# Performance work log

Measured on AMD Instinct MI355X. Metric: run time of the kernel, lower is better.

The kernel has to match this reference:

```python
import jax, jax.numpy as jnp
import numpy as np

B, H, W, C = 4, 256, 256, 256
WS = 8          # window size (both dims)
HEADS = 1
SEQ = WS * WS   # 64 tokens per window
NW = B * (H // WS) * (W // WS)  # 4096 windows
INNER = C * HEADS


def setup_inputs() -> dict:
    key = jax.random.key(0)
    k1, k2, k3, k4 = jax.random.split(key, 4)
    x = jax.random.normal(k1, (B, H, W, C), dtype=jnp.float32)
    attn = jax.random.uniform(k2, (NW, HEADS, SEQ, SEQ), dtype=jnp.float32)
    # to_v: Linear(dim, inner_dim, bias=False); stored as [in, out] for x @ Wv
    Wv = jax.random.normal(k3, (C, INNER), dtype=jnp.float32) * (C ** -0.5)
    # to_out: Linear(inner_dim, dim)
    Wo = jax.random.normal(k4, (INNER, C), dtype=jnp.float32) * (INNER ** -0.5)
    bo = jnp.zeros((C,), dtype=jnp.float32)
    return {"x": x, "attn": attn, "Wv": Wv, "Wo": Wo, "bo": bo}


def reference(x, attn, Wv, Wo, bo):
    b, h, w, c = x.shape
    nh, nw = h // WS, w // WS
    # window partition: b (h b0) (w b1) c -> (b h w) (b0 b1) c
    xw = x.reshape(b, nh, WS, nw, WS, c).transpose(0, 1, 3, 2, 4, 5)
    xw = xw.reshape(b * nh * nw, SEQ, c)
    # value projection, split heads: n s (h d) -> n h s d
    v = (xw @ Wv).reshape(-1, SEQ, HEADS, c).transpose(0, 2, 1, 3)
    # precomputed-attention weighted sum
    out = jnp.einsum('nhij,nhjd->nhid', attn, v)
    # merge heads: n h s d -> n s (h d)
    out = out.transpose(0, 2, 1, 3).reshape(-1, SEQ, HEADS * c)
    out = out @ Wo + bo
    # window un-partition: (b h w) (b0 b1) c -> b (h b0) (w b1) c
    out = out.reshape(b, nh, nw, WS, WS, c).transpose(0, 1, 3, 2, 4, 5)
    return out.reshape(b, h, w, c)
```

## Files before the change

### kernel.cpp

```cpp
#include <hip/hip_runtime.h>
#include <hip/hip_bf16.h>


typedef __bf16 bf16x8 __attribute__((ext_vector_type(8)));
typedef __bf16 bf16x4 __attribute__((ext_vector_type(4)));
typedef float  f32x16 __attribute__((ext_vector_type(16)));
typedef float  f32x4  __attribute__((ext_vector_type(4)));
typedef unsigned int uint;
typedef uint   uint4v __attribute__((ext_vector_type(4)));

#define MFMA32(a, b, c) __builtin_amdgcn_mfma_f32_32x32x16_bf16(a, b, c, 0, 0, 0)

__global__ void wfuse_kernel(const float* __restrict__ Wv,
                             const float* __restrict__ Wo,
                             __bf16* __restrict__ WT) {
  const int n = blockIdx.x;
  const int k = threadIdx.x;
  const float* wvrow = Wv + k * 256;
  float acc = 0.f;
#pragma unroll 4
  for (int j = 0; j < 256; j += 4) {
    f32x4 wv = *(const f32x4*)(wvrow + j);
    acc += wv.x * Wo[(j + 0) * 256 + n];
    acc += wv.y * Wo[(j + 1) * 256 + n];
    acc += wv.z * Wo[(j + 2) * 256 + n];
    acc += wv.w * Wo[(j + 3) * 256 + n];
  }
  WT[n * 256 + k] = (__bf16)acc;
}

static __device__ __forceinline__ uint pkbf(float lo, float hi) {
  return (uint)__builtin_bit_cast(unsigned short, (__bf16)lo) |
         ((uint)__builtin_bit_cast(unsigned short, (__bf16)hi) << 16);
}

static __device__ __forceinline__ void build_bfrags(const f32x16 acc, int lh,
                                                    bf16x8* bf) {
  uint wd0 = pkbf(acc[0],  acc[1]);
  uint wd1 = pkbf(acc[2],  acc[3]);
  uint wd2 = pkbf(acc[4],  acc[5]);
  uint wd3 = pkbf(acc[6],  acc[7]);
  uint wd4 = pkbf(acc[8],  acc[9]);
  uint wd5 = pkbf(acc[10], acc[11]);
  uint wd6 = pkbf(acc[12], acc[13]);
  uint wd7 = pkbf(acc[14], acc[15]);
  {
    uint o0 = (uint)__shfl_xor((int)wd2, 32);
    uint o1 = (uint)__shfl_xor((int)wd3, 32);
    uint o2 = (uint)__shfl_xor((int)wd0, 32);
    uint o3 = (uint)__shfl_xor((int)wd1, 32);
    uint4v uv = { lh ? o0 : wd0, lh ? o1 : wd1,
                  lh ? wd2 : o2, lh ? wd3 : o3 };
    bf[0] = __builtin_bit_cast(bf16x8, uv);
  }
  {
    uint o0 = (uint)__shfl_xor((int)wd6, 32);
    uint o1 = (uint)__shfl_xor((int)wd7, 32);
    uint o2 = (uint)__shfl_xor((int)wd4, 32);
    uint o3 = (uint)__shfl_xor((int)wd5, 32);
    uint4v uv = { lh ? o0 : wd4, lh ? o1 : wd5,
                  lh ? wd6 : o2, lh ? wd7 : o3 };
    bf[1] = __builtin_bit_cast(bf16x8, uv);
  }
}

static __device__ __forceinline__ long wbase(int w) {
  int wi = w & 31;
  int hi = (w >> 5) & 31;
  int b  = w >> 10;
  return (((long)(b * 256 + hi * 8)) * 256 + wi * 8) * 256;
}

__global__ __launch_bounds__(512)
__attribute__((amdgpu_waves_per_eu(4, 4)))
void na_msa_kernel(const float* __restrict__ x,
                   const float* __restrict__ attn,
                   const __bf16* __restrict__ WT,
                   const float* __restrict__ bo,
                   float* __restrict__ out) {
  __shared__ char lds[81920];

  const int t    = threadIdx.x;
  const int lane = t & 63;
  const int wvi  = t >> 6;
  const int ln31 = lane & 31;
  const int lh   = lane >> 5;

  const int tq   = t >> 6;
  const int xch0 = (t & 63) * 4;
  const int arow0 = t >> 4;
  const int ak0  = (t & 15) * 4;

  const __bf16* wtp = WT + (wvi * 32 + ln31) * 256 + 8 * lh;
  const float bv = bo[wvi * 32 + ln31];

  const int w0 = blockIdx.x * 4;

#define XBYT(J)  ((((J) * 8 + tq) * 512) + ((xch0 * 2) ^ (((((J) * 8 + tq)) & 31) << 4)))
#define ABYT(I)  (((I) * 32 + arow0) * 128 + ((ak0 * 2) ^ ((((I) * 32 + arow0) & 7) << 4)))
#define CVT4(V)  bf16x4{ (__bf16)(V).x, (__bf16)(V).y, (__bf16)(V).z, (__bf16)(V).w }

  {
    const float* xp = x + wbase(w0);
    const float* ap = attn + (long)w0 * 4096;
    f32x4 v0 = *(const f32x4*)(xp + 0 * 65536 + t * 4);
    f32x4 v1 = *(const f32x4*)(xp + 1 * 65536 + t * 4);
    f32x4 v2 = *(const f32x4*)(xp + 2 * 65536 + t * 4);
    f32x4 v3 = *(const f32x4*)(xp + 3 * 65536 + t * 4);
    f32x4 v4 = *(const f32x4*)(xp + 4 * 65536 + t * 4);
    f32x4 v5 = *(const f32x4*)(xp + 5 * 65536 + t * 4);
    f32x4 v6 = *(const f32x4*)(xp + 6 * 65536 + t * 4);
    f32x4 v7 = *(const f32x4*)(xp + 7 * 65536 + t * 4);
    f32x4 a0 = *(const f32x4*)(ap + t * 4);
    f32x4 a1 = *(const f32x4*)(ap + (512 + t) * 4);
    *(bf16x4*)(lds + XBYT(0)) = CVT4(v0);
    *(bf16x4*)(lds + XBYT(1)) = CVT4(v1);
    *(bf16x4*)(lds + XBYT(2)) = CVT4(v2);
    *(bf16x4*)(lds + XBYT(3)) = CVT4(v3);
    *(bf16x4*)(lds + XBYT(4)) = CVT4(v4);
    *(bf16x4*)(lds + XBYT(5)) = CVT4(v5);
    *(bf16x4*)(lds + XBYT(6)) = CVT4(v6);
    *(bf16x4*)(lds + XBYT(7)) = CVT4(v7);
    *(bf16x4*)(lds + 32768 + ABYT(0)) = CVT4(a0);
    *(bf16x4*)(lds + 32768 + ABYT(1)) = CVT4(a1);
  }
  asm volatile("s_waitcnt lgkmcnt(0)" ::: "memory");
  __builtin_amdgcn_s_barrier();
  __builtin_amdgcn_sched_barrier(0);

#pragma unroll 1
  for (int i = 0; i < 4; ++i) {
    const int w = w0 + i;
    char* lds_xw = lds + (i & 1) * 40960;
    char* lds_at = lds_xw + 32768;

    f32x4 px0, px1, px2, px3, px4, px5, px6, px7, pa0, pa1;
    if (i < 3) {
      const float* xp = x + wbase(w + 1);
      const float* ap = attn + (long)(w + 1) * 4096;
      px0 = *(const f32x4*)(xp + 0 * 65536 + t * 4);
      px1 = *(const f32x4*)(xp + 1 * 65536 + t * 4);
      px2 = *(const f32x4*)(xp + 2 * 65536 + t * 4);
      px3 = *(const f32x4*)(xp + 3 * 65536 + t * 4);
      px4 = *(const f32x4*)(xp + 4 * 65536 + t * 4);
      px5 = *(const f32x4*)(xp + 5 * 65536 + t * 4);
      px6 = *(const f32x4*)(xp + 6 * 65536 + t * 4);
      px7 = *(const f32x4*)(xp + 7 * 65536 + t * 4);
      pa0 = *(const f32x4*)(ap + t * 4);
      pa1 = *(const f32x4*)(ap + (512 + t) * 4);
    }
    __builtin_amdgcn_sched_barrier(0);

    f32x16 acc0 = {}, acc1 = {};
#pragma unroll 2
    for (int ks = 0; ks < 16; ++ks) {
      int kk = ks * 16 + 8 * lh;
      int byt0 = ln31 * 512 + ((kk * 2) ^ (ln31 << 4));
      bf16x8 a0 = *(const bf16x8*)(lds_xw + byt0);
      bf16x8 a1 = *(const bf16x8*)(lds_xw + byt0 + 16384);
      bf16x8 b0 = *(const bf16x8*)(wtp + ks * 16);
      acc0 = MFMA32(a0, b0, acc0);
      acc1 = MFMA32(a1, b0, acc1);
    }
    __builtin_amdgcn_sched_barrier(0);

    bf16x8 bfr[4];
    build_bfrags(acc0, lh, &bfr[0]);
    build_bfrags(acc1, lh, &bfr[2]);

    if (i < 3) {
      char* bxw = lds + ((i + 1) & 1) * 40960;
      char* bat = bxw + 32768;
      *(bf16x4*)(bxw + XBYT(0)) = CVT4(px0);
      *(bf16x4*)(bxw + XBYT(1)) = CVT4(px1);
      *(bf16x4*)(bxw + XBYT(2)) = CVT4(px2);
      *(bf16x4*)(bxw + XBYT(3)) = CVT4(px3);
      *(bf16x4*)(bxw + XBYT(4)) = CVT4(px4);
      *(bf16x4*)(bxw + XBYT(5)) = CVT4(px5);
      *(bf16x4*)(bxw + XBYT(6)) = CVT4(px6);
      *(bf16x4*)(bxw + XBYT(7)) = CVT4(px7);
      *(bf16x4*)(bat + ABYT(0)) = CVT4(pa0);
      *(bf16x4*)(bat + ABYT(1)) = CVT4(pa1);
    }

    f32x16 o0 = {}, o1 = {};
#pragma unroll
    for (int ks = 0; ks < 4; ++ks) {
      int kk = ks * 16 + 8 * lh;
      int ab0 = ln31 * 128 + ((kk * 2) ^ ((ln31 & 7) << 4));
      bf16x8 a0 = *(const bf16x8*)(lds_at + ab0);
      bf16x8 a1 = *(const bf16x8*)(lds_at + ab0 + 4096);
      o0 = MFMA32(a0, bfr[ks], o0);
      o1 = MFMA32(a1, bfr[ks], o1);
    }

    {
      float* op = out + wbase(w);
      const int ch = wvi * 32 + ln31;
#pragma unroll
      for (int r = 0; r < 16; ++r) {
        int tok = (r & 3) + 8 * (r >> 2) + 4 * lh;
        op[(tok >> 3) * 65536 + (tok & 7) * 256 + ch] = o0[r] + bv;
      }
#pragma unroll
      for (int r = 0; r < 16; ++r) {
        int tok = 32 + (r & 3) + 8 * (r >> 2) + 4 * lh;
        op[(tok >> 3) * 65536 + (tok & 7) * 256 + ch] = o1[r] + bv;
      }
    }

    asm volatile("s_waitcnt lgkmcnt(0)" ::: "memory");
    __builtin_amdgcn_s_barrier();
    __builtin_amdgcn_sched_barrier(0);
  }
}

extern "C" void kernel_launch(void* const* d_in, const int* in_sizes, int n_in,
                              void* d_out, int out_size, void* d_ws, size_t ws_size,
                              hipStream_t stream) {
  const float* x    = (const float*)d_in[0];
  const float* attn = (const float*)d_in[1];
  const float* Wv   = (const float*)d_in[2];
  const float* Wo   = (const float*)d_in[3];
  const float* bo   = (const float*)d_in[4];
  float* out = (float*)d_out;
  __bf16* WT = (__bf16*)d_ws;

  wfuse_kernel<<<256, 256, 0, stream>>>(Wv, Wo, WT);
  na_msa_kernel<<<1024, 512, 0, stream>>>(x, attn, WT, bo, out);
}
```

Before: 180.9 us.

## Hoist fused weights into registers and process 16 windows per block

```diff
diff --git a/kernel.cpp b/kernel.cpp
--- a/kernel.cpp
+++ b/kernel.cpp
@@ -71,8 +71,7 @@
   return (((long)(b * 256 + hi * 8)) * 256 + wi * 8) * 256;
 }
 
-__global__ __launch_bounds__(512)
-__attribute__((amdgpu_waves_per_eu(4, 4)))
+__global__ __launch_bounds__(512, 2)
 void na_msa_kernel(const float* __restrict__ x,
                    const float* __restrict__ attn,
                    const __bf16* __restrict__ WT,
@@ -86,19 +85,30 @@
   const int ln31 = lane & 31;
   const int lh   = lane >> 5;
 
+  const __bf16* wtp = WT + (wvi * 32 + ln31) * 256 + 8 * lh;
+  const float bv = bo[wvi * 32 + ln31];
+
   const int tq   = t >> 6;
   const int xch0 = (t & 63) * 4;
   const int arow0 = t >> 4;
-  const int ak0  = (t & 15) * 4;
-
-  const __bf16* wtp = WT + (wvi * 32 + ln31) * 256 + 8 * lh;
-  const float bv = bo[wvi * 32 + ln31];
-
-  const int w0 = blockIdx.x * 4;
-
-#define XBYT(J)  ((((J) * 8 + tq) * 512) + ((xch0 * 2) ^ (((((J) * 8 + tq)) & 31) << 4)))
-#define ABYT(I)  (((I) * 32 + arow0) * 128 + ((ak0 * 2) ^ ((((I) * 32 + arow0) & 7) << 4)))
+  const int ak0   = (t & 15) * 4;
+
+  const int w0 = blockIdx.x * 16;
+
+#define XBYT(J)  ((((J) * 8 + tq) * 512) + ((xch0 * 2) ^ ((((J) * 8 + tq) & 31) << 4)))
 #define CVT4(V)  bf16x4{ (__bf16)(V).x, (__bf16)(V).y, (__bf16)(V).z, (__bf16)(V).w }
+
+#define AWR(BAT, R0, R1) do {                                              \
+    *(bf16x4*)((BAT) + arow0 * 128 + ((ak0 * 2) ^ ((arow0 & 7) << 4))) =   \
+        bf16x4{ (__bf16)(R0).x, (__bf16)(R0).y, (__bf16)(R0).z, (__bf16)(R0).w }; \
+    int row1_ = 32 + arow0;                                                \
+    *(bf16x4*)((BAT) + row1_ * 128 + ((ak0 * 2) ^ ((row1_ & 7) << 4))) =   \
+        bf16x4{ (__bf16)(R1).x, (__bf16)(R1).y, (__bf16)(R1).z, (__bf16)(R1).w }; \
+    } while (0)
+
+  bf16x8 wb[16];
+#pragma unroll
+  for (int ks = 0; ks < 16; ++ks) wb[ks] = *(const bf16x8*)(wtp + ks * 16);
 
   {
     const float* xp = x + wbase(w0);
@@ -121,21 +131,20 @@
     *(bf16x4*)(lds + XBYT(5)) = CVT4(v5);
     *(bf16x4*)(lds + XBYT(6)) = CVT4(v6);
     *(bf16x4*)(lds + XBYT(7)) = CVT4(v7);
-    *(bf16x4*)(lds + 32768 + ABYT(0)) = CVT4(a0);
-    *(bf16x4*)(lds + 32768 + ABYT(1)) = CVT4(a1);
+    AWR(lds + 32768, a0, a1);
   }
   asm volatile("s_waitcnt lgkmcnt(0)" ::: "memory");
   __builtin_amdgcn_s_barrier();
   __builtin_amdgcn_sched_barrier(0);
 
 #pragma unroll 1
-  for (int i = 0; i < 4; ++i) {
+  for (int i = 0; i < 16; ++i) {
     const int w = w0 + i;
-    char* lds_xw = lds + (i & 1) * 40960;
-    char* lds_at = lds_xw + 32768;
+    const char* xs = lds + (i & 1) * 40960;
+    const char* as = xs + 32768;
 
     f32x4 px0, px1, px2, px3, px4, px5, px6, px7, pa0, pa1;
-    if (i < 3) {
+    if (i < 15) {
       const float* xp = x + wbase(w + 1);
       const float* ap = attn + (long)(w + 1) * 4096;
       px0 = *(const f32x4*)(xp + 0 * 65536 + t * 4);
@@ -152,25 +161,56 @@
     __builtin_amdgcn_sched_barrier(0);
 
     f32x16 acc0 = {}, acc1 = {};
-#pragma unroll 2
+#pragma unroll
     for (int ks = 0; ks < 16; ++ks) {
       int kk = ks * 16 + 8 * lh;
       int byt0 = ln31 * 512 + ((kk * 2) ^ (ln31 << 4));
-      bf16x8 a0 = *(const bf16x8*)(lds_xw + byt0);
-      bf16x8 a1 = *(const bf16x8*)(lds_xw + byt0 + 16384);
-      bf16x8 b0 = *(const bf16x8*)(wtp + ks * 16);
-      acc0 = MFMA32(a0, b0, acc0);
-      acc1 = MFMA32(a1, b0, acc1);
-    }
-    __builtin_amdgcn_sched_barrier(0);
+      bf16x8 a0 = *(const bf16x8*)(xs + byt0);
+      bf16x8 a1 = *(const bf16x8*)(xs + byt0 + 16384);
+      acc0 = MFMA32(a0, wb[ks], acc0);
+      acc1 = MFMA32(a1, wb[ks], acc1);
+    }
 
     bf16x8 bfr[4];
     build_bfrags(acc0, lh, &bfr[0]);
     build_bfrags(acc1, lh, &bfr[2]);
 
-    if (i < 3) {
+    float* op = out + wbase(w);
+    const int ch = wvi * 32 + ln31;
+
+    {
+      f32x16 o0 = {};
+#pragma unroll
+      for (int ks = 0; ks < 4; ++ks) {
+        int kk = ks * 16 + 8 * lh;
+        int ab0 = ln31 * 128 + ((kk * 2) ^ ((ln31 & 7) << 4));
+        bf16x8 a0 = *(const bf16x8*)(as + ab0);
+        o0 = MFMA32(a0, bfr[ks], o0);
+      }
+#pragma unroll
+      for (int r = 0; r < 16; ++r) {
+        int tok = (r & 3) + 8 * (r >> 2) + 4 * lh;
+        op[(tok >> 3) * 65536 + (tok & 7) * 256 + ch] = o0[r] + bv;
+      }
+    }
+    {
+      f32x16 o1 = {};
+#pragma unroll
+      for (int ks = 0; ks < 4; ++ks) {
+        int kk = ks * 16 + 8 * lh;
+        int ab0 = ln31 * 128 + ((kk * 2) ^ ((ln31 & 7) << 4));
+        bf16x8 a1 = *(const bf16x8*)(as + ab0 + 4096);
+        o1 = MFMA32(a1, bfr[ks], o1);
+      }
+#pragma unroll
+      for (int r = 0; r < 16; ++r) {
+        int tok = 32 + (r & 3) + 8 * (r >> 2) + 4 * lh;
+        op[(tok >> 3) * 65536 + (tok & 7) * 256 + ch] = o1[r] + bv;
+      }
+    }
+
+    if (i < 15) {
       char* bxw = lds + ((i + 1) & 1) * 40960;
-      char* bat = bxw + 32768;
       *(bf16x4*)(bxw + XBYT(0)) = CVT4(px0);
       *(bf16x4*)(bxw + XBYT(1)) = CVT4(px1);
       *(bf16x4*)(bxw + XBYT(2)) = CVT4(px2);
@@ -179,40 +219,16 @@
       *(bf16x4*)(bxw + XBYT(5)) = CVT4(px5);
       *(bf16x4*)(bxw + XBYT(6)) = CVT4(px6);
       *(bf16x4*)(bxw + XBYT(7)) = CVT4(px7);
-      *(bf16x4*)(bat + ABYT(0)) = CVT4(pa0);
-      *(bf16x4*)(bat + ABYT(1)) = CVT4(pa1);
-    }
-
-    f32x16 o0 = {}, o1 = {};
-#pragma unroll
-    for (int ks = 0; ks < 4; ++ks) {
-      int kk = ks * 16 + 8 * lh;
-      int ab0 = ln31 * 128 + ((kk * 2) ^ ((ln31 & 7) << 4));
-      bf16x8 a0 = *(const bf16x8*)(lds_at + ab0);
-      bf16x8 a1 = *(const bf16x8*)(lds_at + ab0 + 4096);
-      o0 = MFMA32(a0, bfr[ks], o0);
-      o1 = MFMA32(a1, bfr[ks], o1);
-    }
-
-    {
-      float* op = out + wbase(w);
-      const int ch = wvi * 32 + ln31;
-#pragma unroll
-      for (int r = 0; r < 16; ++r) {
-        int tok = (r & 3) + 8 * (r >> 2) + 4 * lh;
-        op[(tok >> 3) * 65536 + (tok & 7) * 256 + ch] = o0[r] + bv;
-      }
-#pragma unroll
-      for (int r = 0; r < 16; ++r) {
-        int tok = 32 + (r & 3) + 8 * (r >> 2) + 4 * lh;
-        op[(tok >> 3) * 65536 + (tok & 7) * 256 + ch] = o1[r] + bv;
-      }
+      AWR(bxw + 32768, pa0, pa1);
     }
 
     asm volatile("s_waitcnt lgkmcnt(0)" ::: "memory");
     __builtin_amdgcn_s_barrier();
     __builtin_amdgcn_sched_barrier(0);
   }
+#undef XBYT
+#undef CVT4
+#undef AWR
 }
 
 extern "C" void kernel_launch(void* const* d_in, const int* in_sizes, int n_in,
@@ -227,5 +243,5 @@
   __bf16* WT = (__bf16*)d_ws;
 
   wfuse_kernel<<<256, 256, 0, stream>>>(Wv, Wo, WT);
-  na_msa_kernel<<<1024, 512, 0, stream>>>(x, attn, WT, bo, out);
-}
+  na_msa_kernel<<<256, 512, 0, stream>>>(x, attn, WT, bo, out);
+}
```

Result: faster. 153.2 us (-15.3%).
